# Optimization experiments

Measured on AMD Instinct MI355X. Metric: run time of the kernel, lower is better.

Reference implementation:

```python
import jax, jax.numpy as jnp
import numpy as np

DIM = 512
HEADS = 8


def setup_inputs() -> dict:
    key = jax.random.key(0)
    k1, k2, k3, k4 = jax.random.split(key, 4)
    head_dim = DIM // HEADS
    scale = head_dim ** -0.5
    x = jax.random.normal(k1, (4, 4096, DIM), dtype=jnp.float32)
    Wqkv = jax.random.normal(k2, (3 * DIM, DIM), dtype=jnp.float32) * (DIM ** -0.5)
    temperature = jnp.ones((HEADS, 1, 1), dtype=jnp.float32) * scale
    Wproj = jax.random.normal(k3, (DIM, DIM), dtype=jnp.float32) * (DIM ** -0.5)
    bproj = jnp.zeros((DIM,), dtype=jnp.float32)
    return {"x": x, "Wqkv": Wqkv, "temperature": temperature, "Wproj": Wproj, "bproj": bproj}


def reference(x, Wqkv, temperature, Wproj, bproj):
    B, N, C = x.shape
    H = temperature.shape[0]
    D = C // H
    qkv = (x @ Wqkv.T).reshape(B, N, 3, H, D).transpose(2, 0, 3, 1, 4)  # (3,B,H,N,D)
    q, k, v = qkv[0], qkv[1], qkv[2]
    q = jax.nn.relu(q)
    k = jax.nn.relu(k)
    # denom = clamp(q @ sum_n k, min=100) -> (B,H,N,1)
    ksum = k.sum(axis=2)  # (B,H,D)
    denom = jnp.clip(jnp.einsum('bhnd,bhd->bhn', q, ksum), 100.0)[..., None]
    # attn = (k^T v) * temperature -> (B,H,D,D)
    attn = jnp.einsum('bhnd,bhne->bhde', k, v) * temperature
    attn1 = jnp.einsum('bhnd,bhde->bhne', q, attn)  # (B,H,N,D)
    out = attn1 / denom
    y = out.transpose(0, 2, 1, 3).reshape(B, N, C) @ Wproj.T + bproj
    return (y, attn1)
```

## Files before the change

### kernel.cpp

```cpp
#include <hip/hip_runtime.h>
#include <cstdint>
#include <cstddef>

typedef _Float16 f16;
typedef _Float16 f16x4 __attribute__((ext_vector_type(4)));
typedef _Float16 f16x8 __attribute__((ext_vector_type(8)));
typedef float f32x4 __attribute__((ext_vector_type(4)));

#define MFMA16(a, b, c) __builtin_amdgcn_mfma_f32_16x16x32_f16(a, b, c, 0, 0, 0)

static __device__ __forceinline__ void gld16(const void* g, void* l) {
  __builtin_amdgcn_global_load_lds(
      (const __attribute__((address_space(1))) void*)g,
      (__attribute__((address_space(3))) void*)l, 16, 0, 0);
}

#define B_ 4
#define N_ 4096
#define C_ 512
#define H_ 8
#define D_ 64
#define BN_ROWS 16384
#define QKV_COLS 1536

__global__ __launch_bounds__(256) void k_convert(
    const float* __restrict__ x, const float* __restrict__ wqkv,
    const float* __restrict__ wproj,
    f16* __restrict__ xh, f16* __restrict__ wqkvh, f16* __restrict__ wprojh)
{
  const int NX  = (BN_ROWS * C_) / 4;
  const int NW1 = (QKV_COLS * C_) / 4;
  const int NW2 = (C_ * C_) / 4;
  const int total = NX + NW1 + NW2;
  const int stride = gridDim.x * blockDim.x;
  for (int i = blockIdx.x * blockDim.x + threadIdx.x; i < total; i += stride) {
    const float4* s; f16x4* d; int j;
    if (i < NX)              { s = (const float4*)x;     d = (f16x4*)xh;     j = i; }
    else if (i < NX + NW1)   { s = (const float4*)wqkv;  d = (f16x4*)wqkvh;  j = i - NX; }
    else                     { s = (const float4*)wproj; d = (f16x4*)wprojh; j = i - NX - NW1; }
    float4 v = s[j];
    f16x4 o; o[0] = (f16)v.x; o[1] = (f16)v.y; o[2] = (f16)v.z; o[3] = (f16)v.w;
    d[j] = o;
  }
}

__global__ __launch_bounds__(256) void k_qkv_gemm(
    const f16* __restrict__ X, const f16* __restrict__ W, f16* __restrict__ Out)
{
  __shared__ f16 As[128][64];
  __shared__ f16 Bs[128][64];
  int w = (blockIdx.x & 7) * 192 + (blockIdx.x >> 3);
  const int n0 = (w % 12) * 128;
  const int m0 = (w / 12) * 128;
  const int tid = threadIdx.x;
  const int wid = tid >> 6;
  const int lane = tid & 63;
  const int lr = lane & 15, lg = lane >> 4;
  const int sr = lane >> 3;
  const int sslot = (lane & 7) ^ sr;
  const int wr = (wid >> 1) * 64, wc = (wid & 1) * 64;
  f32x4 acc[4][4] = {};
  for (int kt = 0; kt < 512; kt += 64) {
#pragma unroll
    for (int i = 0; i < 4; ++i) {
      int chunk = wid * 4 + i;
      int row = chunk * 8 + sr;
      gld16(&X[(size_t)(m0 + row) * 512 + kt + sslot * 8], &As[chunk * 8][0]);
      gld16(&W[(size_t)(n0 + row) * 512 + kt + sslot * 8], &Bs[chunk * 8][0]);
    }
    __syncthreads();
#pragma unroll
    for (int kk = 0; kk < 2; ++kk) {
      f16x8 af[4], bf[4];
#pragma unroll
      for (int m = 0; m < 4; ++m)
        af[m] = *(const f16x8*)&As[wr + m * 16 + lr][(((kk * 4 + lg) ^ (lr & 7)) * 8)];
#pragma unroll
      for (int n = 0; n < 4; ++n)
        bf[n] = *(const f16x8*)&Bs[wc + n * 16 + lr][(((kk * 4 + lg) ^ (lr & 7)) * 8)];
#pragma unroll
      for (int m = 0; m < 4; ++m)
#pragma unroll
        for (int n = 0; n < 4; ++n)
          acc[m][n] = MFMA16(bf[n], af[m], acc[m][n]);
    }
    __syncthreads();
  }
#pragma unroll
  for (int m = 0; m < 4; ++m)
#pragma unroll
    for (int n = 0; n < 4; ++n) {
      int row = m0 + wr + m * 16 + lr;
      int col = n0 + wc + n * 16 + lg * 4;
      f16x4 o;
      bool relu = (col < 1024);
#pragma unroll
      for (int j = 0; j < 4; ++j) {
        float v = acc[m][n][j];
        if (relu) v = fmaxf(v, 0.f);
        o[j] = (f16)v;
      }
      *(f16x4*)&Out[(size_t)row * QKV_COLS + col] = o;
    }
}

__global__ __launch_bounds__(256) void k_ktv(
    const f16* __restrict__ qkv, float* __restrict__ partial, float* __restrict__ pksum)
{
  __shared__ f16 ks[32][64];
  __shared__ f16 vs[32][64];
  const int bh = blockIdx.x, sp = blockIdx.y;
  const int b = bh >> 3, h = bh & 7;
  const int tid = threadIdx.x, wid = tid >> 6, lane = tid & 63;
  const int srow = lane >> 3, scol = (lane & 7) * 8;
  const int td = (wid << 2) | (lane >> 4);
  const int te = lane & 15;
  float acc[4][4] = {};
  float ksacc[4] = {0.f, 0.f, 0.f, 0.f};
  const size_t rowbase = (size_t)b * N_ + sp * 128;
  for (int t = 0; t < 4; ++t) {
    int nb = t * 32 + wid * 8 + srow;
    gld16(&qkv[(rowbase + nb) * QKV_COLS + 512 + h * 64 + scol], &ks[wid * 8][0]);
    gld16(&qkv[(rowbase + nb) * QKV_COLS + 1024 + h * 64 + scol], &vs[wid * 8][0]);
    __syncthreads();
#pragma unroll 4
    for (int n = 0; n < 32; ++n) {
      f16x4 kd = *(const f16x4*)&ks[n][td * 4];
      f16x4 ve = *(const f16x4*)&vs[n][te * 4];
      float kf[4], vf[4];
#pragma unroll
      for (int i = 0; i < 4; ++i) { kf[i] = (float)kd[i]; vf[i] = (float)ve[i]; }
#pragma unroll
      for (int i = 0; i < 4; ++i)
#pragma unroll
        for (int j = 0; j < 4; ++j)
          acc[i][j] += kf[i] * vf[j];
      if (te == 0) {
#pragma unroll
        for (int i = 0; i < 4; ++i) ksacc[i] += kf[i];
      }
    }
    __syncthreads();
  }
  float* pp = partial + (size_t)(bh * 32 + sp) * 4096;
#pragma unroll
  for (int i = 0; i < 4; ++i)
#pragma unroll
    for (int j = 0; j < 4; ++j)
      pp[(td * 4 + i) * 64 + te * 4 + j] = acc[i][j];
  if (te == 0) {
    float* kp = pksum + (bh * 32 + sp) * 64;
#pragma unroll
    for (int i = 0; i < 4; ++i) kp[td * 4 + i] = ksacc[i];
  }
}

__global__ __launch_bounds__(256) void k_reduce(
    const float* __restrict__ partial, const float* __restrict__ pksum,
    float* __restrict__ attn_acc, float* __restrict__ ksum)
{
  const int bh = blockIdx.x, seg = blockIdx.y, tid = threadIdx.x;
  const int i = seg * 256 + tid;
  float s = 0.f;
#pragma unroll 8
  for (int sp = 0; sp < 32; ++sp) s += partial[(size_t)(bh * 32 + sp) * 4096 + i];
  attn_acc[bh * 4096 + i] = s;
  if (seg == 0 && tid < 64) {
    float t2 = 0.f;
#pragma unroll 8
    for (int sp = 0; sp < 32; ++sp) t2 += pksum[(bh * 32 + sp) * 64 + tid];
    ksum[bh * 64 + tid] = t2;
  }
}

__global__ __launch_bounds__(256, 1) void k_attn_proj(
    const f16* __restrict__ qkv, const float* __restrict__ attn_acc,
    const float* __restrict__ ksum, const float* __restrict__ temp,
    const f16* __restrict__ Wp, const float* __restrict__ bias,
    float* __restrict__ attn1_out, float* __restrict__ Y)
{
  __shared__ f16 attnT[64][64];
  __shared__ f16 qs[64][64];
  __shared__ f16 outs[64][512];
  __shared__ f16 Bs[2][256][64];
  __shared__ float ksum_s[512];
  __shared__ float bias_s[512];
  __shared__ float denom_s[64];

  const int bid = blockIdx.x;
  const int b = bid >> 6, sp = bid & 63;
  const size_t gr = (size_t)b * N_ + sp * 64;
  const int tid = threadIdx.x;
  const int wid = tid >> 6, lane = tid & 63;
  const int lr = lane & 15, lg = lane >> 4;
  const int sr = lane >> 3, sslot = (lane & 7) ^ sr;

  ksum_s[tid]       = ksum[b * 512 + tid];
  ksum_s[tid + 256] = ksum[b * 512 + tid + 256];
  bias_s[tid]       = bias[tid];
  bias_s[tid + 256] = bias[tid + 256];

  for (int h = 0; h < 8; ++h) {
    const float tsc = temp[h];
    {
      int e = tid & 63, dblk = (tid >> 6) * 16;
      float vals[16];
#pragma unroll
      for (int x = 0; x < 16; ++x)
        vals[x] = attn_acc[(size_t)(b * 8 + h) * 4096 + (dblk + x) * 64 + e] * tsc;
#pragma unroll
      for (int half = 0; half < 2; ++half) {
        int slot = ((dblk >> 3) + half) ^ (e & 7);
        f16x8 pk;
#pragma unroll
        for (int j = 0; j < 8; ++j) pk[j] = (f16)vals[half * 8 + j];
        *(f16x8*)&attnT[e][slot * 8] = pk;
      }
    }
#pragma unroll
    for (int rr = 0; rr < 2; ++rr) {
      int row = rr * 32 + wid * 8;
      gld16(&qkv[(gr + row + sr) * QKV_COLS + h * 64 + sslot * 8], &qs[row][0]);
    }
    __syncthreads();
    if (tid < 64) {
      int r = tid;
      float dot = 0.f;
#pragma unroll
      for (int c = 0; c < 8; ++c) {
        f16x8 qv = *(const f16x8*)&qs[r][((c ^ (r & 7)) * 8)];
#pragma unroll
        for (int j = 0; j < 8; ++j) dot += (float)qv[j] * ksum_s[h * 64 + c * 8 + j];
      }
      denom_s[r] = fmaxf(dot, 100.f);
    }
    const int arow = wid * 16 + lr;
    f16x8 af[2], bf[4][2];
#pragma unroll
    for (int kk = 0; kk < 2; ++kk)
      af[kk] = *(const f16x8*)&qs[arow][(((kk * 4 + lg) ^ (lr & 7)) * 8)];
#pragma unroll
    for (int et = 0; et < 4; ++et)
#pragma unroll
      for (int kk = 0; kk < 2; ++kk)
        bf[et][kk] = *(const f16x8*)&attnT[et * 16 + lr][(((kk * 4 + lg) ^ (lr & 7)) * 8)];
    f32x4 acc1[4] = {};
#pragma unroll
    for (int kk = 0; kk < 2; ++kk)
#pragma unroll
      for (int et = 0; et < 4; ++et)
        acc1[et] = MFMA16(bf[et][kk], af[kk], acc1[et]);
    __syncthreads();
    {
      const int rl = wid * 16 + lr;
      const float dn = denom_s[rl];
#pragma unroll
      for (int et = 0; et < 4; ++et) {
        int e = et * 16 + lg * 4;
        float4 o;
        o.x = acc1[et][0]; o.y = acc1[et][1]; o.z = acc1[et][2]; o.w = acc1[et][3];
        *(float4*)&attn1_out[((size_t)(b * 8 + h) * N_ + sp * 64 + rl) * 64 + e] = o;
        f16x4 oh;
#pragma unroll
        for (int j = 0; j < 4; ++j) oh[j] = (f16)(acc1[et][j] / dn);
        int c = h * 64 + e;
        *(f16x4*)((char*)&outs[0][0] + rl * 1024 +
                  (((c >> 3) ^ (rl & 7)) * 16) + (lg & 1) * 8) = oh;
      }
    }
  }
  __syncthreads();

  f32x4 accP0[4][4] = {};
  f32x4 accP1[4][4] = {};

#define STAGEP(hf_, kc_, bufi)                                                \
  do {                                                                        \
    _Pragma("unroll")                                                         \
    for (int rd = 0; rd < 8; ++rd) {                                          \
      int row = rd * 32 + wid * 8;                                            \
      gld16(&Wp[(size_t)((hf_) * 256 + row + sr) * 512 + (kc_) * 64 + sslot * 8], \
            &Bs[bufi][row][0]);                                               \
    }                                                                         \
  } while (0)

  STAGEP(0, 0, 0);
  __syncthreads();

  for (int kc = 0; kc < 8; ++kc) {
    STAGEP(1, kc, 1);
    f16x8 afp[2][4];
#pragma unroll
    for (int kk = 0; kk < 2; ++kk)
#pragma unroll
      for (int m = 0; m < 4; ++m) {
        int row = m * 16 + lr;
        afp[kk][m] = *(const f16x8*)((const char*)&outs[0][0] + row * 1024 +
                      (((kc * 8 + kk * 4 + lg) ^ (row & 7)) * 16));
      }
    {
      f16x8 bfp[4];
#pragma unroll
      for (int kk = 0; kk < 2; ++kk) {
#pragma unroll
        for (int n = 0; n < 4; ++n)
          bfp[n] = *(const f16x8*)&Bs[0][wid * 64 + n * 16 + lr][(((kk * 4 + lg) ^ (lr & 7)) * 8)];
#pragma unroll
        for (int m = 0; m < 4; ++m)
#pragma unroll
          for (int n = 0; n < 4; ++n)
            accP0[m][n] = MFMA16(bfp[n], afp[kk][m], accP0[m][n]);
      }
    }
    __syncthreads();
    if (kc < 7) STAGEP(0, kc + 1, 0);
    {
      f16x8 bfp[4];
#pragma unroll
      for (int kk = 0; kk < 2; ++kk) {
#pragma unroll
        for (int n = 0; n < 4; ++n)
          bfp[n] = *(const f16x8*)&Bs[1][wid * 64 + n * 16 + lr][(((kk * 4 + lg) ^ (lr & 7)) * 8)];
#pragma unroll
        for (int m = 0; m < 4; ++m)
#pragma unroll
          for (int n = 0; n < 4; ++n)
            accP1[m][n] = MFMA16(bfp[n], afp[kk][m], accP1[m][n]);
      }
    }
    __syncthreads();
  }
#undef STAGEP

#pragma unroll
  for (int m = 0; m < 4; ++m)
#pragma unroll
    for (int n = 0; n < 4; ++n) {
      size_t row = gr + m * 16 + lr;
      int col0 = wid * 64 + n * 16 + lg * 4;
      float4 o0;
      o0.x = accP0[m][n][0] + bias_s[col0 + 0];
      o0.y = accP0[m][n][1] + bias_s[col0 + 1];
      o0.z = accP0[m][n][2] + bias_s[col0 + 2];
      o0.w = accP0[m][n][3] + bias_s[col0 + 3];
      *(float4*)&Y[row * C_ + col0] = o0;
      int col1 = col0 + 256;
      float4 o1;
      o1.x = accP1[m][n][0] + bias_s[col1 + 0];
      o1.y = accP1[m][n][1] + bias_s[col1 + 1];
      o1.z = accP1[m][n][2] + bias_s[col1 + 2];
      o1.w = accP1[m][n][3] + bias_s[col1 + 3];
      *(float4*)&Y[row * C_ + col1] = o1;
    }
}

extern "C" void kernel_launch(void* const* d_in, const int* in_sizes, int n_in,
                              void* d_out, int out_size, void* d_ws, size_t ws_size,
                              hipStream_t stream)
{
  const float* x     = (const float*)d_in[0];
  const float* wqkv  = (const float*)d_in[1];
  const float* temp  = (const float*)d_in[2];
  const float* wproj = (const float*)d_in[3];
  const float* bproj = (const float*)d_in[4];
  float* y_out     = (float*)d_out;
  float* attn1_out = (float*)d_out + 8388608;

  char* ws = (char*)d_ws;
  f16*   xh       = (f16*)(ws);
  float* partial  = (float*)(ws);
  f16*   wqkvh    = (f16*)(ws + 16777216);
  f16*   wprojh   = (f16*)(ws + 18350080);
  f16*   qkvh     = (f16*)(ws + 18874368);
  float* attn_acc = (float*)(ws + 69206016);
  float* ksum     = (float*)(ws + 69730304);
  float* pksum    = (float*)(ws + 69738496);

  hipLaunchKernelGGL(k_convert,   dim3(2048),   dim3(256), 0, stream, x, wqkv, wproj, xh, wqkvh, wprojh);
  hipLaunchKernelGGL(k_qkv_gemm,  dim3(1536),   dim3(256), 0, stream, xh, wqkvh, qkvh);
  hipLaunchKernelGGL(k_ktv,       dim3(32, 32), dim3(256), 0, stream, qkvh, partial, pksum);
  hipLaunchKernelGGL(k_reduce,    dim3(32, 16), dim3(256), 0, stream, partial, pksum, attn_acc, ksum);
  hipLaunchKernelGGL(k_attn_proj, dim3(256),    dim3(256), 0, stream,
                     qkvh, attn_acc, ksum, temp, wprojh, bproj, attn1_out, y_out);
}
```

Measured before the change: 121.2 us.

## Double-buffer QKV GEMM LDS tiles with 256x128 blocks and 8 waves

Rewrites the QKV projection GEMM to double-buffer the LDS tiles. The next K-slice is issued via global_load_lds while MFMAs run on the current one, with one barrier per iteration instead of two. Block tile grows to 256x128 with 512 threads (8 waves, each still computing 64x64), halving the grid to 768 blocks. It also raises wave priority around the MFMA bursts. This doubles LDS use to 96KB, which limits occupancy to one block per CU, and it relies on manual waitcnt and sched_barrier control.

After: 122.8 us. Within noise of the previous version (+1.3%).

```diff
diff --git a/kernel.cpp b/kernel.cpp
--- a/kernel.cpp
+++ b/kernel.cpp
@@ -44,54 +44,96 @@
   }
 }
 
-__global__ __launch_bounds__(256) void k_qkv_gemm(
+__global__ __launch_bounds__(512, 1) void k_qkv_gemm(
     const f16* __restrict__ X, const f16* __restrict__ W, f16* __restrict__ Out)
 {
-  __shared__ f16 As[128][64];
-  __shared__ f16 Bs[128][64];
-  int w = (blockIdx.x & 7) * 192 + (blockIdx.x >> 3);
+  __shared__ f16 As[2][256][64];
+  __shared__ f16 Bs[2][128][64];
+  int w = (blockIdx.x & 7) * 96 + (blockIdx.x >> 3);
+  const int m0 = (w / 12) * 256;
   const int n0 = (w % 12) * 128;
-  const int m0 = (w / 12) * 128;
   const int tid = threadIdx.x;
-  const int wid = tid >> 6;
-  const int lane = tid & 63;
+  const int wid = tid >> 6, lane = tid & 63;
   const int lr = lane & 15, lg = lane >> 4;
-  const int sr = lane >> 3;
-  const int sslot = (lane & 7) ^ sr;
-  const int wr = (wid >> 1) * 64, wc = (wid & 1) * 64;
+  const int wm = wid >> 1, wn = wid & 1;
+  const int sr = lane >> 3, sslot = (lane & 7) ^ sr;
   f32x4 acc[4][4] = {};
-  for (int kt = 0; kt < 512; kt += 64) {
-#pragma unroll
-    for (int i = 0; i < 4; ++i) {
-      int chunk = wid * 4 + i;
-      int row = chunk * 8 + sr;
-      gld16(&X[(size_t)(m0 + row) * 512 + kt + sslot * 8], &As[chunk * 8][0]);
-      gld16(&W[(size_t)(n0 + row) * 512 + kt + sslot * 8], &Bs[chunk * 8][0]);
-    }
-    __syncthreads();
-#pragma unroll
-    for (int kk = 0; kk < 2; ++kk) {
+
+#define STAGE(tt, s)                                                          \
+  do {                                                                        \
+    _Pragma("unroll")                                                         \
+    for (int i = 0; i < 4; ++i) {                                             \
+      int chunk = wid * 4 + i;                                                \
+      gld16(&X[(size_t)(m0 + chunk * 8 + sr) * 512 + (tt) * 64 + sslot * 8],  \
+            &As[s][chunk * 8][0]);                                            \
+    }                                                                         \
+    _Pragma("unroll")                                                         \
+    for (int i = 0; i < 2; ++i) {                                             \
+      int chunk = wid * 2 + i;                                                \
+      gld16(&W[(size_t)(n0 + chunk * 8 + sr) * 512 + (tt) * 64 + sslot * 8],  \
+            &Bs[s][chunk * 8][0]);                                            \
+    }                                                                         \
+  } while (0)
+
+  STAGE(0, 0);
+  asm volatile("s_waitcnt vmcnt(0)" ::: "memory");
+  __builtin_amdgcn_s_barrier();
+  asm volatile("" ::: "memory");
+
+#pragma unroll
+  for (int t = 0; t < 8; ++t) {
+    const int p = t & 1, q = p ^ 1;
+    if (t < 7) STAGE(t + 1, q);
+    {
       f16x8 af[4], bf[4];
 #pragma unroll
       for (int m = 0; m < 4; ++m)
-        af[m] = *(const f16x8*)&As[wr + m * 16 + lr][(((kk * 4 + lg) ^ (lr & 7)) * 8)];
+        af[m] = *(const f16x8*)&As[p][wm * 64 + m * 16 + lr][((lg ^ (lr & 7)) * 8)];
 #pragma unroll
       for (int n = 0; n < 4; ++n)
-        bf[n] = *(const f16x8*)&Bs[wc + n * 16 + lr][(((kk * 4 + lg) ^ (lr & 7)) * 8)];
+        bf[n] = *(const f16x8*)&Bs[p][wn * 64 + n * 16 + lr][((lg ^ (lr & 7)) * 8)];
+      asm volatile("s_waitcnt lgkmcnt(0)" ::: "memory");
+      __builtin_amdgcn_sched_barrier(0);
+      __builtin_amdgcn_s_setprio(1);
 #pragma unroll
       for (int m = 0; m < 4; ++m)
 #pragma unroll
         for (int n = 0; n < 4; ++n)
           acc[m][n] = MFMA16(bf[n], af[m], acc[m][n]);
-    }
-    __syncthreads();
-  }
+      __builtin_amdgcn_s_setprio(0);
+    }
+    {
+      f16x8 af[4], bf[4];
+#pragma unroll
+      for (int m = 0; m < 4; ++m)
+        af[m] = *(const f16x8*)&As[p][wm * 64 + m * 16 + lr][((((4 + lg)) ^ (lr & 7)) * 8)];
+#pragma unroll
+      for (int n = 0; n < 4; ++n)
+        bf[n] = *(const f16x8*)&Bs[p][wn * 64 + n * 16 + lr][((((4 + lg)) ^ (lr & 7)) * 8)];
+      asm volatile("s_waitcnt lgkmcnt(0)" ::: "memory");
+      __builtin_amdgcn_sched_barrier(0);
+      __builtin_amdgcn_s_setprio(1);
+#pragma unroll
+      for (int m = 0; m < 4; ++m)
+#pragma unroll
+        for (int n = 0; n < 4; ++n)
+          acc[m][n] = MFMA16(bf[n], af[m], acc[m][n]);
+      __builtin_amdgcn_s_setprio(0);
+    }
+    if (t < 7) {
+      asm volatile("s_waitcnt vmcnt(0)" ::: "memory");
+      __builtin_amdgcn_s_barrier();
+      asm volatile("" ::: "memory");
+    }
+  }
+#undef STAGE
+
 #pragma unroll
   for (int m = 0; m < 4; ++m)
 #pragma unroll
     for (int n = 0; n < 4; ++n) {
-      int row = m0 + wr + m * 16 + lr;
-      int col = n0 + wc + n * 16 + lg * 4;
+      int row = m0 + wm * 64 + m * 16 + lr;
+      int col = n0 + wn * 64 + n * 16 + lg * 4;
       f16x4 o;
       bool relu = (col < 1024);
 #pragma unroll
@@ -377,7 +419,7 @@
   float* pksum    = (float*)(ws + 69738496);
 
   hipLaunchKernelGGL(k_convert,   dim3(2048),   dim3(256), 0, stream, x, wqkv, wproj, xh, wqkvh, wprojh);
-  hipLaunchKernelGGL(k_qkv_gemm,  dim3(1536),   dim3(256), 0, stream, xh, wqkvh, qkvh);
+  hipLaunchKernelGGL(k_qkv_gemm,  dim3(768),    dim3(512), 0, stream, xh, wqkvh, qkvh);
   hipLaunchKernelGGL(k_ktv,       dim3(32, 32), dim3(256), 0, stream, qkvh, partial, pksum);
   hipLaunchKernelGGL(k_reduce,    dim3(32, 16), dim3(256), 0, stream, partial, pksum, attn_acc, ksum);
   hipLaunchKernelGGL(k_attn_proj, dim3(256),    dim3(256), 0, stream,
```

## Give each wave its own head in attn stage and halve ktv splits

Applied to the files above, without the earlier changes.

The attention stage of k_attn_proj now has each of the four waves handle a whole head (two rounds of four heads). This replaces eight sequential head iterations, each with block-wide barriers, and uses explicit vmcnt waits instead. The attnT/qs buffers are unioned with the projection staging buffer to keep LDS usage bounded. Separately, k_ktv processes 256 rows per block with 16 splits instead of 32, which halves the partial-sum traffic and the work in k_reduce but launches fewer blocks.

Result: faster. 116.6 us (-3.9%).

```diff
diff --git a/kernel.cpp b/kernel.cpp
--- a/kernel.cpp
+++ b/kernel.cpp
@@ -117,8 +117,8 @@
   const int te = lane & 15;
   float acc[4][4] = {};
   float ksacc[4] = {0.f, 0.f, 0.f, 0.f};
-  const size_t rowbase = (size_t)b * N_ + sp * 128;
-  for (int t = 0; t < 4; ++t) {
+  const size_t rowbase = (size_t)b * N_ + sp * 256;
+  for (int t = 0; t < 8; ++t) {
     int nb = t * 32 + wid * 8 + srow;
     gld16(&qkv[(rowbase + nb) * QKV_COLS + 512 + h * 64 + scol], &ks[wid * 8][0]);
     gld16(&qkv[(rowbase + nb) * QKV_COLS + 1024 + h * 64 + scol], &vs[wid * 8][0]);
@@ -142,14 +142,14 @@
     }
     __syncthreads();
   }
-  float* pp = partial + (size_t)(bh * 32 + sp) * 4096;
+  float* pp = partial + (size_t)(bh * 16 + sp) * 4096;
 #pragma unroll
   for (int i = 0; i < 4; ++i)
 #pragma unroll
     for (int j = 0; j < 4; ++j)
       pp[(td * 4 + i) * 64 + te * 4 + j] = acc[i][j];
   if (te == 0) {
-    float* kp = pksum + (bh * 32 + sp) * 64;
+    float* kp = pksum + (bh * 16 + sp) * 64;
 #pragma unroll
     for (int i = 0; i < 4; ++i) kp[td * 4 + i] = ksacc[i];
   }
@@ -163,12 +163,12 @@
   const int i = seg * 256 + tid;
   float s = 0.f;
 #pragma unroll 8
-  for (int sp = 0; sp < 32; ++sp) s += partial[(size_t)(bh * 32 + sp) * 4096 + i];
+  for (int sp = 0; sp < 16; ++sp) s += partial[(size_t)(bh * 16 + sp) * 4096 + i];
   attn_acc[bh * 4096 + i] = s;
   if (seg == 0 && tid < 64) {
     float t2 = 0.f;
 #pragma unroll 8
-    for (int sp = 0; sp < 32; ++sp) t2 += pksum[(bh * 32 + sp) * 64 + tid];
+    for (int sp = 0; sp < 16; ++sp) t2 += pksum[(bh * 16 + sp) * 64 + tid];
     ksum[bh * 64 + tid] = t2;
   }
 }
@@ -179,13 +179,14 @@
     const f16* __restrict__ Wp, const float* __restrict__ bias,
     float* __restrict__ attn1_out, float* __restrict__ Y)
 {
-  __shared__ f16 attnT[64][64];
-  __shared__ f16 qs[64][64];
   __shared__ f16 outs[64][512];
-  __shared__ f16 Bs[2][256][64];
+  __shared__ union {
+    struct { f16 attnT[4][64][64]; f16 qs[4][64][64]; } a;
+    f16 Bs[2][256][64];
+  } u;
   __shared__ float ksum_s[512];
   __shared__ float bias_s[512];
-  __shared__ float denom_s[64];
+  __shared__ float denom_s[4][64];
 
   const int bid = blockIdx.x;
   const int b = bid >> 6, sp = bid & 63;
@@ -199,70 +200,75 @@
   ksum_s[tid + 256] = ksum[b * 512 + tid + 256];
   bias_s[tid]       = bias[tid];
   bias_s[tid + 256] = bias[tid + 256];
-
-  for (int h = 0; h < 8; ++h) {
+  __syncthreads();
+
+#pragma unroll
+  for (int bi = 0; bi < 2; ++bi) {
+    const int h = bi * 4 + wid;
     const float tsc = temp[h];
+#pragma unroll
+    for (int rr = 0; rr < 8; ++rr)
+      gld16(&qkv[(gr + rr * 8 + sr) * QKV_COLS + h * 64 + sslot * 8],
+            &u.a.qs[wid][rr * 8][0]);
+#pragma unroll
+    for (int dc = 0; dc < 4; ++dc) {
+      float vals[16];
+#pragma unroll
+      for (int x = 0; x < 16; ++x)
+        vals[x] = attn_acc[(size_t)(b * 8 + h) * 4096 + (dc * 16 + x) * 64 + lane] * tsc;
+#pragma unroll
+      for (int half = 0; half < 2; ++half) {
+        int slot = (dc * 2 + half) ^ (lane & 7);
+        f16x8 pk;
+#pragma unroll
+        for (int j = 0; j < 8; ++j) pk[j] = (f16)vals[half * 8 + j];
+        *(f16x8*)&u.a.attnT[wid][lane][slot * 8] = pk;
+      }
+    }
+    asm volatile("s_waitcnt vmcnt(0)" ::: "memory");
     {
-      int e = tid & 63, dblk = (tid >> 6) * 16;
-      float vals[16];
-#pragma unroll
-      for (int x = 0; x < 16; ++x)
-        vals[x] = attn_acc[(size_t)(b * 8 + h) * 4096 + (dblk + x) * 64 + e] * tsc;
-#pragma unroll
-      for (int half = 0; half < 2; ++half) {
-        int slot = ((dblk >> 3) + half) ^ (e & 7);
-        f16x8 pk;
-#pragma unroll
-        for (int j = 0; j < 8; ++j) pk[j] = (f16)vals[half * 8 + j];
-        *(f16x8*)&attnT[e][slot * 8] = pk;
-      }
-    }
-#pragma unroll
-    for (int rr = 0; rr < 2; ++rr) {
-      int row = rr * 32 + wid * 8;
-      gld16(&qkv[(gr + row + sr) * QKV_COLS + h * 64 + sslot * 8], &qs[row][0]);
-    }
-    __syncthreads();
-    if (tid < 64) {
-      int r = tid;
+      const int r = lane;
       float dot = 0.f;
 #pragma unroll
       for (int c = 0; c < 8; ++c) {
-        f16x8 qv = *(const f16x8*)&qs[r][((c ^ (r & 7)) * 8)];
+        f16x8 qv = *(const f16x8*)&u.a.qs[wid][r][((c ^ (r & 7)) * 8)];
 #pragma unroll
         for (int j = 0; j < 8; ++j) dot += (float)qv[j] * ksum_s[h * 64 + c * 8 + j];
       }
-      denom_s[r] = fmaxf(dot, 100.f);
-    }
-    const int arow = wid * 16 + lr;
-    f16x8 af[2], bf[4][2];
+      denom_s[wid][r] = fmaxf(dot, 100.f);
+    }
+    f16x8 af[2][4], bf[4][2];
 #pragma unroll
     for (int kk = 0; kk < 2; ++kk)
-      af[kk] = *(const f16x8*)&qs[arow][(((kk * 4 + lg) ^ (lr & 7)) * 8)];
+#pragma unroll
+      for (int m = 0; m < 4; ++m)
+        af[kk][m] = *(const f16x8*)&u.a.qs[wid][m * 16 + lr][(((kk * 4 + lg) ^ (lr & 7)) * 8)];
 #pragma unroll
     for (int et = 0; et < 4; ++et)
 #pragma unroll
       for (int kk = 0; kk < 2; ++kk)
-        bf[et][kk] = *(const f16x8*)&attnT[et * 16 + lr][(((kk * 4 + lg) ^ (lr & 7)) * 8)];
-    f32x4 acc1[4] = {};
+        bf[et][kk] = *(const f16x8*)&u.a.attnT[wid][et * 16 + lr][(((kk * 4 + lg) ^ (lr & 7)) * 8)];
+    f32x4 acc1[4][4] = {};
 #pragma unroll
     for (int kk = 0; kk < 2; ++kk)
 #pragma unroll
-      for (int et = 0; et < 4; ++et)
-        acc1[et] = MFMA16(bf[et][kk], af[kk], acc1[et]);
-    __syncthreads();
-    {
-      const int rl = wid * 16 + lr;
-      const float dn = denom_s[rl];
+      for (int m = 0; m < 4; ++m)
+#pragma unroll
+        for (int et = 0; et < 4; ++et)
+          acc1[m][et] = MFMA16(bf[et][kk], af[kk][m], acc1[m][et]);
+#pragma unroll
+    for (int m = 0; m < 4; ++m) {
+      const int rl = m * 16 + lr;
+      const float dn = denom_s[wid][rl];
 #pragma unroll
       for (int et = 0; et < 4; ++et) {
         int e = et * 16 + lg * 4;
         float4 o;
-        o.x = acc1[et][0]; o.y = acc1[et][1]; o.z = acc1[et][2]; o.w = acc1[et][3];
+        o.x = acc1[m][et][0]; o.y = acc1[m][et][1]; o.z = acc1[m][et][2]; o.w = acc1[m][et][3];
         *(float4*)&attn1_out[((size_t)(b * 8 + h) * N_ + sp * 64 + rl) * 64 + e] = o;
         f16x4 oh;
 #pragma unroll
-        for (int j = 0; j < 4; ++j) oh[j] = (f16)(acc1[et][j] / dn);
+        for (int j = 0; j < 4; ++j) oh[j] = (f16)(acc1[m][et][j] / dn);
         int c = h * 64 + e;
         *(f16x4*)((char*)&outs[0][0] + rl * 1024 +
                   (((c >> 3) ^ (rl & 7)) * 16) + (lg & 1) * 8) = oh;
@@ -280,7 +286,7 @@
     for (int rd = 0; rd < 8; ++rd) {                                          \
       int row = rd * 32 + wid * 8;                                            \
       gld16(&Wp[(size_t)((hf_) * 256 + row + sr) * 512 + (kc_) * 64 + sslot * 8], \
-            &Bs[bufi][row][0]);                                               \
+            &u.Bs[bufi][row][0]);                                             \
     }                                                                         \
   } while (0)
 
@@ -304,7 +310,7 @@
       for (int kk = 0; kk < 2; ++kk) {
 #pragma unroll
         for (int n = 0; n < 4; ++n)
-          bfp[n] = *(const f16x8*)&Bs[0][wid * 64 + n * 16 + lr][(((kk * 4 + lg) ^ (lr & 7)) * 8)];
+          bfp[n] = *(const f16x8*)&u.Bs[0][wid * 64 + n * 16 + lr][(((kk * 4 + lg) ^ (lr & 7)) * 8)];
 #pragma unroll
         for (int m = 0; m < 4; ++m)
 #pragma unroll
@@ -320,7 +326,7 @@
       for (int kk = 0; kk < 2; ++kk) {
 #pragma unroll
         for (int n = 0; n < 4; ++n)
-          bfp[n] = *(const f16x8*)&Bs[1][wid * 64 + n * 16 + lr][(((kk * 4 + lg) ^ (lr & 7)) * 8)];
+          bfp[n] = *(const f16x8*)&u.Bs[1][wid * 64 + n * 16 + lr][(((kk * 4 + lg) ^ (lr & 7)) * 8)];
 #pragma unroll
         for (int m = 0; m < 4; ++m)
 #pragma unroll
@@ -378,7 +384,7 @@
 
   hipLaunchKernelGGL(k_convert,   dim3(2048),   dim3(256), 0, stream, x, wqkv, wproj, xh, wqkvh, wprojh);
   hipLaunchKernelGGL(k_qkv_gemm,  dim3(1536),   dim3(256), 0, stream, xh, wqkvh, qkvh);
-  hipLaunchKernelGGL(k_ktv,       dim3(32, 32), dim3(256), 0, stream, qkvh, partial, pksum);
+  hipLaunchKernelGGL(k_ktv,       dim3(32, 16), dim3(256), 0, stream, qkvh, partial, pksum);
   hipLaunchKernelGGL(k_reduce,    dim3(32, 16), dim3(256), 0, stream, partial, pksum, attn_acc, ksum);
   hipLaunchKernelGGL(k_attn_proj, dim3(256),    dim3(256), 0, stream,
                      qkvh, attn_acc, ksum, temp, wprojh, bproj, attn1_out, y_out);
```
